# Kernel optimization log

Hardware: AMD Instinct MI355X
Metric: run time of the kernel (lower is better)

Reference implementation:

```python
import math
import jax, jax.numpy as jnp
import numpy as np
from jax import lax

SQRT2 = 1.4142135623730951
EPS = 1e-8


def _make_kernel():
    k = jnp.array([1.0, 3.0, 3.0, 1.0], jnp.float32)
    k = k[None, :] * k[:, None]
    return k / k.sum()  # [4,4], sums to 1


def _blur(x, kernel, pad, up=1):
    # upfirdn2d: optional zero-insertion upsample, pad, FIR filter (depthwise conv)
    C = x.shape[1]
    rhs = jnp.broadcast_to(kernel[None, None], (C, 1, kernel.shape[0], kernel.shape[1]))
    p0, p1 = pad
    if up > 1:
        p1 = p1 + (up - 1)  # zero-insertion appends up-1 trailing zeros per axis
    return lax.conv_general_dilated(
        x, rhs, (1, 1), [(p0, p1), (p0, p1)], lhs_dilation=(up, up),
        dimension_numbers=('NCHW', 'OIHW', 'NCHW'), feature_group_count=C)


def _mod_linear(style, mw, mb):
    # EqualLinear: scale = 1/sqrt(in_dim)
    scale = 1.0 / math.sqrt(mw.shape[1])
    return style @ (mw * scale).T + mb


def _mod_weight(w, s, demodulate):
    # w: [O,I,kh,kw], s: [B,I] -> per-sample weights [B,O,I,kh,kw]
    scale = 1.0 / math.sqrt(w.shape[1] * w.shape[2] * w.shape[3])
    wb = scale * w[None] * s[:, None, :, None, None]
    if demodulate:
        d = lax.rsqrt(jnp.sum(wb * wb, axis=(2, 3, 4)) + EPS)
        wb = wb * d[:, :, None, None, None]
    return wb


def _per_sample_conv(x, wb, padding):
    def f(xi, wi):
        return lax.conv_general_dilated(
            xi[None], wi, (1, 1), [(padding, padding)] * 2,
            dimension_numbers=('NCHW', 'OIHW', 'NCHW'))[0]
    return jax.vmap(f)(x, wb)


def _per_sample_conv_transpose2(x, wb):
    # torch conv_transpose2d(stride=2, pad=0) == lhs-dilated conv with flipped kernel
    k = wb.shape[-1]
    def f(xi, wi):
        return lax.conv_general_dilated(
            xi[None], jnp.flip(wi, (2, 3)), (1, 1), [(k - 1, k - 1)] * 2,
            lhs_dilation=(2, 2), dimension_numbers=('NCHW', 'OIHW', 'NCHW'))[0]
    return jax.vmap(f)(x, wb)


def _fused_lrelu(x, b):
    return jax.nn.leaky_relu(x + b[None, :, None, None], 0.2) * SQRT2


def setup_inputs() -> dict:
    key = jax.random.key(0)
    ks = jax.random.split(key, 16)
    B, C, H, S = 8, 512, 32, 512
    return {
        'x': jax.random.normal(ks[0], (B, C, H, H), jnp.float32),
        'style': jax.random.normal(ks[1], (B, S), jnp.float32),
        'skip_rgb': jax.random.normal(ks[2], (B, 3, H, H), jnp.float32),
        'noise1': jax.random.normal(ks[3], (B, 1, 2 * H, 2 * H), jnp.float32),
        'noise2': jax.random.normal(ks[4], (B, 1, 2 * H, 2 * H), jnp.float32),
        'w1': jax.random.normal(ks[5], (C, C, 3, 3), jnp.float32),
        'mod1_w': jax.random.normal(ks[6], (C, S), jnp.float32),
        'mod1_b': jnp.ones((C,), jnp.float32),
        'bias1': jnp.zeros((C,), jnp.float32),
        'noise1_w': 0.1 * jnp.ones((1,), jnp.float32),
        'w2': jax.random.normal(ks[7], (C, C, 3, 3), jnp.float32),
        'mod2_w': jax.random.normal(ks[8], (C, S), jnp.float32),
        'mod2_b': jnp.ones((C,), jnp.float32),
        'bias2': jnp.zeros((C,), jnp.float32),
        'noise2_w': 0.1 * jnp.ones((1,), jnp.float32),
        'w3': jax.random.normal(ks[9], (3, C, 1, 1), jnp.float32),
        'mod3_w': jax.random.normal(ks[10], (C, S), jnp.float32),
        'mod3_b': jnp.ones((C,), jnp.float32),
        'bias3': jnp.zeros((3,), jnp.float32),
    }


def reference(x, style, skip_rgb, noise1, noise2,
              w1, mod1_w, mod1_b, bias1, noise1_w,
              w2, mod2_w, mod2_b, bias2, noise2_w,
              w3, mod3_w, mod3_b, bias3):
    kernel = _make_kernel()
    # --- StyledConv with upsample: modulated conv_transpose + blur + noise + fused lrelu
    s1 = _mod_linear(style, mod1_w, mod1_b)            # [B, Cin]
    wb1 = _mod_weight(w1, s1, True)                    # [B, O, I, 3, 3]
    out = _per_sample_conv_transpose2(x, wb1)          # [B, O, 2H+1, 2W+1]
    out = _blur(out, kernel * 4.0, (1, 1))             # [B, O, 2H, 2W]
    out = out + noise1_w[0] * noise1
    out = _fused_lrelu(out, bias1)
    # --- StyledConv, same resolution
    s2 = _mod_linear(style, mod2_w, mod2_b)
    wb2 = _mod_weight(w2, s2, True)
    out = _per_sample_conv(out, wb2, 1)
    out = out + noise2_w[0] * noise2
    out = _fused_lrelu(out, bias2)
    # --- ToRGB: 1x1 modulated conv (no demodulation) + bias + upsampled skip
    s3 = _mod_linear(style, mod3_w, mod3_b)
    wb3 = _mod_weight(w3, s3, False)
    rgb = _per_sample_conv(out, wb3, 0) + bias3[None, :, None, None]
    skip = _blur(skip_rgb, kernel * 4.0, (2, 1), up=2)  # Upsample(factor=2)
    return rgb + skip
```

## Files before the change

### kernel.cpp

```cpp
#include <hip/hip_runtime.h>

typedef _Float16 f16;
typedef __attribute__((ext_vector_type(4))) _Float16 f16x4;
typedef __attribute__((ext_vector_type(8))) _Float16 f16x8;
typedef __attribute__((ext_vector_type(4))) float f32x4;

#define SC_CONV 0.014731391274719738f
#define SC_RGB  0.04419417382415922f
#define SC_LIN  0.04419417382415922f
#define SQRT2F  1.4142135623730951f

__device__ inline f32x4 zero_f32x4() {
    f32x4 v;
    #pragma unroll
    for (int i = 0; i < 4; ++i) v[i] = 0.0f;
    return v;
}
__device__ inline void gload_lds16(const void* g, void* l) {
    __builtin_amdgcn_global_load_lds(
        (const __attribute__((address_space(1))) unsigned int*)g,
        (__attribute__((address_space(3))) unsigned int*)l, 16, 0, 0);
}

__global__ __launch_bounds__(256) void k_prep1(
    const float* __restrict__ style,
    const float* __restrict__ m1w, const float* __restrict__ m1b,
    const float* __restrict__ m2w, const float* __restrict__ m2b,
    const float* __restrict__ m3w, const float* __restrict__ m3b,
    float* __restrict__ s1, float* __restrict__ s2, float* __restrict__ s3,
    const float* __restrict__ w1, const float* __restrict__ w2,
    f16* __restrict__ wA1, f16* __restrict__ wA2,
    float* __restrict__ wsq1, float* __restrict__ wsq2,
    f16* __restrict__ xmh, f16* __restrict__ in1h, f16* __restrict__ ctp,
    const float* __restrict__ skiprgb, const float* __restrict__ bias3,
    float* __restrict__ out)
{
    const int bx = blockIdx.x;
    if (bx < 2048) {
        int g = bx * 256 + threadIdx.x;
        int set = g >> 18; int oi = g & 262143;
        const float* w = (set ? w2 : w1) + (size_t)oi * 9;
        f16* wa = set ? wA2 : wA1;
        float* wq = set ? wsq2 : wsq1;
        int o = oi >> 9, i = oi & 511;
        float sw = 0.f;
        #pragma unroll
        for (int t = 0; t < 9; ++t) {
            float v = w[t];
            wa[((size_t)t * 512 + o) * 512 + i] = (f16)v;
            sw += v * v;
        }
        wq[oi] = sw;
    } else if (bx < 2432) {
        const int lane = threadIdx.x & 63, wid = threadIdx.x >> 6;
        const int gw = (bx - 2048) * 4 + wid;
        const int set = gw >> 9, o = gw & 511;
        const float* mw = set == 0 ? m1w : set == 1 ? m2w : m3w;
        const float* mb = set == 0 ? m1b : set == 1 ? m2b : m3b;
        float* outp = set == 0 ? s1 : set == 1 ? s2 : s3;
        const float4 m0 = *(const float4*)(mw + (size_t)o * 512 + lane * 8);
        const float4 m1 = *(const float4*)(mw + (size_t)o * 512 + lane * 8 + 4);
        const float mv[8] = {m0.x, m0.y, m0.z, m0.w, m1.x, m1.y, m1.z, m1.w};
        float acc[8];
        #pragma unroll
        for (int b = 0; b < 8; ++b) {
            const float4 sA = *(const float4*)(style + b * 512 + lane * 8);
            const float4 sB = *(const float4*)(style + b * 512 + lane * 8 + 4);
            acc[b] = mv[0]*sA.x + mv[1]*sA.y + mv[2]*sA.z + mv[3]*sA.w
                   + mv[4]*sB.x + mv[5]*sB.y + mv[6]*sB.z + mv[7]*sB.w;
        }
        #pragma unroll
        for (int b = 0; b < 8; ++b)
            #pragma unroll
            for (int off = 1; off < 64; off <<= 1)
                acc[b] += __shfl_xor(acc[b], off);
        if (lane == 0) {
            const float mbv = mb[o];
            #pragma unroll
            for (int b = 0; b < 8; ++b) outp[b * 512 + o] = acc[b] * SC_LIN + mbv;
        }
    } else if (bx < 2448) {
        const int idx = bx - 2432, b = idx & 7, type = idx >> 3;
        f16x8 z;
        #pragma unroll
        for (int i = 0; i < 8; ++i) z[i] = (_Float16)0.0f;
        if (type == 0) {
            for (int j = threadIdx.x; j < 132 * 64; j += 256) {
                int pix = j >> 6, e = j & 63;
                int r, c;
                if (pix < 34)       { r = 0;            c = pix; }
                else if (pix < 68)  { r = 33;           c = pix - 34; }
                else if (pix < 100) { r = pix - 68 + 1; c = 0; }
                else                { r = pix - 100 + 1; c = 33; }
                *(f16x8*)(xmh + ((((size_t)b * 34 + r) * 34 + c) * 512) + e * 8) = z;
            }
        } else {
            for (int j = threadIdx.x; j < 260 * 64; j += 256) {
                int pix = j >> 6, e = j & 63;
                int r, c;
                if (pix < 66)       { r = 0;             c = pix; }
                else if (pix < 132) { r = 65;            c = pix - 66; }
                else if (pix < 196) { r = pix - 132 + 1; c = 0; }
                else                { r = pix - 196 + 1; c = 65; }
                *(f16x8*)(in1h + ((((size_t)b * 66 + r) * 66 + c) * 512) + e * 8) = z;
            }
        }
    } else if (bx < 2456) {
        const int b = bx - 2448;
        f16x8 z;
        #pragma unroll
        for (int i = 0; i < 8; ++i) z[i] = (_Float16)0.0f;
        for (int j = threadIdx.x; j < 266 * 64; j += 256) {
            int pix = j >> 6, e = j & 63;
            int r, c;
            if (pix < 68)       { r = 0;             c = pix; }
            else if (pix < 136) { r = 66;            c = pix - 68; }
            else if (pix < 201) { r = 1 + (pix - 136); c = 0; }
            else                { r = 1 + (pix - 201); c = 66; }
            *(f16x8*)(ctp + ((((size_t)b * 68 + r) * 68 + c) * 512) + e * 8) = z;
        }
    } else {
        const unsigned g = (unsigned)(bx - 2456) * 256 + threadIdx.x;
        const unsigned b = g / 12288u, rem = g - b * 12288u;
        const unsigned c = rem >> 12, pix = rem & 4095u;
        const int y = (int)(pix >> 6), xx = (int)(pix & 63);
        const float kk[4] = {1.f, 3.f, 3.f, 1.f};
        int sy = y & 1, sx = xx & 1;
        int u0 = ((y + sy) >> 1) - 1, v0 = ((xx + sx) >> 1) - 1;
        float cy0 = kk[sy], cy1 = kk[sy + 2], cx0 = kk[sx], cx1 = kk[sx + 2];
        float sk = 0.f;
        #pragma unroll
        for (int aa = 0; aa < 2; ++aa)
            #pragma unroll
            for (int bb = 0; bb < 2; ++bb) {
                int u = u0 + aa, vv = v0 + bb;
                if (u >= 0 && u < 32 && vv >= 0 && vv < 32)
                    sk += (aa ? cy1 : cy0) * (bb ? cx1 : cx0) *
                          skiprgb[(((size_t)b * 3 + c) * 32 + u) * 32 + vv];
            }
        out[(((size_t)b * 3 + c) * 64 + y) * 64 + xx] = bias3[c] + sk * (1.0f / 16.0f);
    }
}

__global__ __launch_bounds__(256) void k_prep2(
    const float* __restrict__ wsq1, const float* __restrict__ s1, float* __restrict__ d1,
    const float* __restrict__ wsq2, const float* __restrict__ s2, float* __restrict__ d2,
    const float* __restrict__ x, f16* __restrict__ xmh)
{
    __shared__ float red[8][4];
    __shared__ float t[32][33];
    const int bx = blockIdx.x;
    if (bx < 1024) {
        const int o = bx & 511, set = bx >> 9;
        const float* wq = set ? wsq2 : wsq1;
        const float* s = set ? s2 : s1;
        float* d = set ? d2 : d1;
        float acc[8] = {0,0,0,0,0,0,0,0};
        for (int i = threadIdx.x; i < 512; i += 256) {
            const float sw = wq[(size_t)o * 512 + i];
            #pragma unroll
            for (int b = 0; b < 8; ++b) { float sv = s[b * 512 + i]; acc[b] += sv * sv * sw; }
        }
        const int lane = threadIdx.x & 63, wid = threadIdx.x >> 6;
        #pragma unroll
        for (int b = 0; b < 8; ++b)
            #pragma unroll
            for (int off = 1; off < 64; off <<= 1)
                acc[b] += __shfl_xor(acc[b], off);
        if (lane == 0) {
            #pragma unroll
            for (int b = 0; b < 8; ++b) red[b][wid] = acc[b];
        }
        __syncthreads();
        if (threadIdx.x < 8) {
            float s4 = red[threadIdx.x][0] + red[threadIdx.x][1] + red[threadIdx.x][2] + red[threadIdx.x][3];
            d[threadIdx.x * 512 + o] = rsqrtf(s4 * (SC_CONV * SC_CONV) + 1e-8f);
        }
    } else {
        const int idx = bx - 1024, u = idx & 31, b = idx >> 5;
        int tx = threadIdx.x & 31, ty = threadIdx.x >> 5;
        for (int ic = 0; ic < 512; ic += 32) {
            #pragma unroll
            for (int k = 0; k < 4; ++k) {
                int i = ic + ty + 8 * k;
                t[ty + 8 * k][tx] = x[(((size_t)b * 512 + i) * 32 + u) * 32 + tx];
            }
            __syncthreads();
            #pragma unroll
            for (int k = 0; k < 4; ++k) {
                int v = ty + 8 * k;
                int i = ic + tx;
                float sv = s1[b * 512 + i] * SC_CONV;
                xmh[(((size_t)b * 34 + u + 1) * 34 + v + 1) * 512 + i] = (f16)(t[tx][v] * sv);
            }
            __syncthreads();
        }
    }
}

__global__ __launch_bounds__(512, 2) void k_conv1m(
    const f16* __restrict__ xmh, const f16* __restrict__ wA1, f16* __restrict__ ctp)
{
    const int gid = blockIdx.x;
    int ph, tbase;
    if (gid < 70)       { ph = 0; tbase = 0; }
    else if (gid < 136) { ph = 1; tbase = 70; }
    else if (gid < 202) { ph = 2; tbase = 136; }
    else                { ph = 3; tbase = 202; }
    const int p = ph >> 1, q = ph & 1;
    const int Nn = q ? 32 : 33;
    const unsigned npos = (unsigned)((p ? 32 : 33) * Nn);
    const unsigned ntot = npos * 8;
    const int tiles_n = (int)((ntot + 255) >> 8);
    int t = gid - tbase;
    const int mB = (t >= tiles_n) ? 256 : 0;
    if (t >= tiles_n) t -= tiles_n;
    const unsigned posB = (unsigned)t * 256;
    const int ntx = q ? 1 : 2;
    const int ntaps = (p ? 1 : 2) * ntx;
    const int ktsteps = ntaps * 8;

    __shared__ f16 LA[2][16384];
    __shared__ f16 LB[2][16384];
    const int tid = threadIdx.x, lane = tid & 63, wid = tid >> 6;
    const int wm = wid >> 2, wn = wid & 3;
    const int lr = lane & 15, lk = lane >> 4;

    f32x4 acc[8][4];
    #pragma unroll
    for (int mf = 0; mf < 8; ++mf)
        #pragma unroll
        for (int nf = 0; nf < 4; ++nf) acc[mf][nf] = zero_f32x4();

    int aoff[4], boff[4], ldst[4];
    #pragma unroll
    for (int c = 0; c < 4; ++c) {
        const int idx = c * 512 + tid;
        const int row = idx >> 3, sl = idx & 7, ssl = sl ^ (row & 7);
        ldst[c] = idx * 16;
        aoff[c] = (mB + row) * 512 + ssl * 8;
        unsigned pos = posB + (unsigned)row;
        if (pos > ntot - 1) pos = ntot - 1;
        const unsigned bb = pos / npos, rr = pos - bb * npos;
        const unsigned u = rr / (unsigned)Nn, v = rr - u * (unsigned)Nn;
        boff[c] = (int)(((bb * 34 + u + 1) * 34 + v + 1) * 512) + ssl * 8;
    }

    int raA[8], raB[4];
    #pragma unroll
    for (int mf = 0; mf < 8; ++mf) {
        const int R = wm * 128 + mf * 16 + lr;
        raA[mf] = R * 128 + ((lk ^ (R & 7)) * 16);
    }
    #pragma unroll
    for (int nf = 0; nf < 4; ++nf) {
        const int R = wn * 64 + nf * 16 + lr;
        raB[nf] = R * 128 + ((lk ^ (R & 7)) * 16);
    }

    auto stageA = [&](int kt, int d) {
        const int tt = kt >> 3, icb = (kt & 7) << 6;
        const int ay = (ntx == 2) ? (tt >> 1) : tt;
        const int ax = (ntx == 2) ? (tt & 1) : 0;
        const f16* base = wA1 + (size_t)((p + 2 * ay) * 3 + (q + 2 * ax)) * 262144 + icb;
        char* dst = (char*)LA[d];
        #pragma unroll
        for (int c = 0; c < 4; ++c)
            gload_lds16(base + aoff[c], dst + ldst[c]);
    };
    auto stageB = [&](int kt, int d) {
        const int tt = kt >> 3, icb = (kt & 7) << 6;
        const int ay = (ntx == 2) ? (tt >> 1) : tt;
        const int ax = (ntx == 2) ? (tt & 1) : 0;
        const f16* base = xmh - (long)(ay * 34 + ax) * 512 + icb;
        char* dst = (char*)LB[d];
        #pragma unroll
        for (int c = 0; c < 4; ++c)
            gload_lds16(base + boff[c], dst + ldst[c]);
    };

    stageB(0, 0);
    stageA(0, 0);
    for (int kt = 0; kt < ktsteps; ++kt) {
        const int d = kt & 1;
        asm volatile("s_waitcnt vmcnt(0)" ::: "memory");
        __builtin_amdgcn_s_barrier();
        const char* A = (const char*)LA[d];
        const char* Bm = (const char*)LB[d];
        f16x8 bf[4][2], af[4][2];
        #pragma unroll
        for (int nf = 0; nf < 4; ++nf) {
            bf[nf][0] = *(const f16x8*)(Bm + raB[nf]);
            bf[nf][1] = *(const f16x8*)(Bm + (raB[nf] ^ 64));
        }
        #pragma unroll
        for (int mf = 0; mf < 4; ++mf) {
            af[mf][0] = *(const f16x8*)(A + raA[mf]);
            af[mf][1] = *(const f16x8*)(A + (raA[mf] ^ 64));
        }
        if (kt + 1 < ktsteps) stageB(kt + 1, d ^ 1);
        asm volatile("s_waitcnt lgkmcnt(0)" ::: "memory");
        __builtin_amdgcn_sched_barrier(0);
        __builtin_amdgcn_s_setprio(1);
        #pragma unroll
        for (int mf = 0; mf < 4; ++mf)
            #pragma unroll
            for (int nf = 0; nf < 4; ++nf) {
                acc[mf][nf] = __builtin_amdgcn_mfma_f32_16x16x32_f16(
                    af[mf][0], bf[nf][0], acc[mf][nf], 0, 0, 0);
                acc[mf][nf] = __builtin_amdgcn_mfma_f32_16x16x32_f16(
                    af[mf][1], bf[nf][1], acc[mf][nf], 0, 0, 0);
            }
        __builtin_amdgcn_s_setprio(0);
        #pragma unroll
        for (int mf = 0; mf < 4; ++mf) {
            af[mf][0] = *(const f16x8*)(A + raA[mf + 4]);
            af[mf][1] = *(const f16x8*)(A + (raA[mf + 4] ^ 64));
        }
        if (kt + 1 < ktsteps) stageA(kt + 1, d ^ 1);
        asm volatile("s_waitcnt lgkmcnt(0)" ::: "memory");
        __builtin_amdgcn_sched_barrier(0);
        __builtin_amdgcn_s_setprio(1);
        #pragma unroll
        for (int mf = 0; mf < 4; ++mf)
            #pragma unroll
            for (int nf = 0; nf < 4; ++nf) {
                acc[mf + 4][nf] = __builtin_amdgcn_mfma_f32_16x16x32_f16(
                    af[mf][0], bf[nf][0], acc[mf + 4][nf], 0, 0, 0);
                acc[mf + 4][nf] = __builtin_amdgcn_mfma_f32_16x16x32_f16(
                    af[mf][1], bf[nf][1], acc[mf + 4][nf], 0, 0, 0);
            }
        __builtin_amdgcn_s_setprio(0);
    }

    #pragma unroll
    for (int nf = 0; nf < 4; ++nf) {
        const int c = wn * 64 + nf * 16 + lr;
        const unsigned pos = posB + (unsigned)c;
        if (pos >= ntot) continue;
        const unsigned bb = pos / npos, rr = pos - bb * npos;
        const unsigned u = rr / (unsigned)Nn, v = rr - u * (unsigned)Nn;
        const int row = 1 + 2 * (int)u + p, col = 1 + 2 * (int)v + q;
        f16* dst = ctp + (((size_t)bb * 68 + row) * 68 + col) * 512;
        #pragma unroll
        for (int mf = 0; mf < 8; ++mf) {
            const int ob = mB + wm * 128 + mf * 16 + lk * 4;
            f16x4 st;
            #pragma unroll
            for (int r = 0; r < 4; ++r) st[r] = (f16)acc[mf][nf][r];
            *(f16x4*)(dst + ob) = st;
        }
    }
}

__global__ __launch_bounds__(256) void k_blur1(
    const f16* __restrict__ ctp, const float* __restrict__ d1,
    const float* __restrict__ noise1, const float* __restrict__ nw1,
    const float* __restrict__ bias1, const float* __restrict__ s2,
    f16* __restrict__ in1h)
{
    const int y0 = blockIdx.x * 2, b = blockIdx.y;
    const int tx = threadIdx.x & 63, xg = threadIdx.x >> 6;
    const int ch = tx * 8, x0 = xg * 16;
    const f16* base = ctp + ((size_t)(b * 68 + y0) * 68) * 512 + ch;

    float d1v[8], b1v[8], s2v[8];
    {
        const float4 a0 = *(const float4*)(d1 + b * 512 + ch);
        const float4 a1 = *(const float4*)(d1 + b * 512 + ch + 4);
        const float4 c0 = *(const float4*)(bias1 + ch);
        const float4 c1 = *(const float4*)(bias1 + ch + 4);
        const float4 e0 = *(const float4*)(s2 + b * 512 + ch);
        const float4 e1 = *(const float4*)(s2 + b * 512 + ch + 4);
        d1v[0]=a0.x; d1v[1]=a0.y; d1v[2]=a0.z; d1v[3]=a0.w;
        d1v[4]=a1.x; d1v[5]=a1.y; d1v[6]=a1.z; d1v[7]=a1.w;
        b1v[0]=c0.x; b1v[1]=c0.y; b1v[2]=c0.z; b1v[3]=c0.w;
        b1v[4]=c1.x; b1v[5]=c1.y; b1v[6]=c1.z; b1v[7]=c1.w;
        s2v[0]=e0.x; s2v[1]=e0.y; s2v[2]=e0.z; s2v[3]=e0.w;
        s2v[4]=e1.x; s2v[5]=e1.y; s2v[6]=e1.z; s2v[7]=e1.w;
    }
    const float nw = nw1[0];
    const float* nrow0 = noise1 + ((size_t)b * 64 + y0) * 64;
    const float* nrow1 = nrow0 + 64;

    float cs[4][2][8];
    #define LOADCOL(cc, slot)                                                   \
        do {                                                                    \
            f16x8 v0 = *(const f16x8*)(base + ((size_t)(0 * 68 + (cc))) * 512); \
            f16x8 v1 = *(const f16x8*)(base + ((size_t)(1 * 68 + (cc))) * 512); \
            f16x8 v2 = *(const f16x8*)(base + ((size_t)(2 * 68 + (cc))) * 512); \
            f16x8 v3 = *(const f16x8*)(base + ((size_t)(3 * 68 + (cc))) * 512); \
            f16x8 v4 = *(const f16x8*)(base + ((size_t)(4 * 68 + (cc))) * 512); \
            _Pragma("unroll")                                                   \
            for (int k = 0; k < 8; ++k) {                                       \
                float f0=(float)v0[k], f1=(float)v1[k], f2=(float)v2[k];        \
                float f3=(float)v3[k], f4=(float)v4[k];                         \
                cs[slot][0][k] = f0 + 3.f*f1 + 3.f*f2 + f3;                     \
                cs[slot][1][k] = f1 + 3.f*f2 + 3.f*f3 + f4;                     \
            }                                                                   \
        } while (0)

    LOADCOL(x0 + 0, 0);
    LOADCOL(x0 + 1, 1);
    LOADCOL(x0 + 2, 2);
    #pragma unroll
    for (int xi = 0; xi < 16; ++xi) {
        LOADCOL(x0 + xi + 3, ((xi + 3) & 3));
        const int x = x0 + xi;
        const float nz0 = nw * nrow0[x];
        const float nz1 = nw * nrow1[x];
        f16x8 st0, st1;
        #pragma unroll
        for (int k = 0; k < 8; ++k) {
            float s0 = (cs[xi & 3][0][k] + cs[(xi + 3) & 3][0][k])
                     + 3.f * (cs[(xi + 1) & 3][0][k] + cs[(xi + 2) & 3][0][k]);
            float v0 = s0 * (1.0f / 16.0f) * d1v[k] + nz0 + b1v[k];
            v0 = (v0 > 0.f ? v0 : 0.2f * v0) * SQRT2F;
            st0[k] = (f16)(v0 * s2v[k] * SC_CONV);
            float s1r = (cs[xi & 3][1][k] + cs[(xi + 3) & 3][1][k])
                      + 3.f * (cs[(xi + 1) & 3][1][k] + cs[(xi + 2) & 3][1][k]);
            float v1 = s1r * (1.0f / 16.0f) * d1v[k] + nz1 + b1v[k];
            v1 = (v1 > 0.f ? v1 : 0.2f * v1) * SQRT2F;
            st1[k] = (f16)(v1 * s2v[k] * SC_CONV);
        }
        *(f16x8*)(in1h + (((size_t)(b * 66 + 1 + y0) * 66) + 1 + x) * 512 + ch) = st0;
        *(f16x8*)(in1h + (((size_t)(b * 66 + 2 + y0) * 66) + 1 + x) * 512 + ch) = st1;
    }
    #undef LOADCOL
}

__global__ __launch_bounds__(512, 2) void k_conv2_8p(
    const f16* __restrict__ in1h, const f16* __restrict__ wA2,
    const float* __restrict__ d2, const float* __restrict__ noise2,
    const float* __restrict__ nw2, const float* __restrict__ bias2,
    const float* __restrict__ s3, const float* __restrict__ w3,
    float* __restrict__ out)
{
    const int b = blockIdx.z, mB = blockIdx.y * 256, nT = blockIdx.x;
    const int y0 = nT * 4;
    __shared__ f16 LA[2][16384];
    __shared__ f16 LB[2][16384];
    const int tid = threadIdx.x, lane = tid & 63, wid = tid >> 6;
    const int wm = wid >> 2, wn = wid & 3;
    const int lr = lane & 15, lk = lane >> 4;

    f32x4 acc[8][4];
    #pragma unroll
    for (int mf = 0; mf < 8; ++mf)
        #pragma unroll
        for (int nf = 0; nf < 4; ++nf) acc[mf][nf] = zero_f32x4();

    int aoff[4], boff[4], ldst[4];
    #pragma unroll
    for (int c = 0; c < 4; ++c) {
        const int idx = c * 512 + tid;
        const int row = idx >> 3, sl = idx & 7, ssl = sl ^ (row & 7);
        ldst[c] = idx * 16;
        aoff[c] = (mB + row) * 512 + ssl * 8;
        const int py = y0 + (row >> 6), px = row & 63;
        boff[c] = ((b * 66 + 1 + py) * 66 + 1 + px) * 512 + ssl * 8;
    }

    int raA[8], raB[4];
    #pragma unroll
    for (int mf = 0; mf < 8; ++mf) {
        const int R = wm * 128 + mf * 16 + lr;
        raA[mf] = R * 128 + ((lk ^ (R & 7)) * 16);
    }
    #pragma unroll
    for (int nf = 0; nf < 4; ++nf) {
        const int R = wn * 64 + nf * 16 + lr;
        raB[nf] = R * 128 + ((lk ^ (R & 7)) * 16);
    }

    auto stageA = [&](int kt, int d) {
        const int tap = kt >> 3, icb = (kt & 7) << 6;
        const f16* base = wA2 + (size_t)tap * 262144 + icb;
        char* dst = (char*)LA[d];
        #pragma unroll
        for (int c = 0; c < 4; ++c)
            gload_lds16(base + aoff[c], dst + ldst[c]);
    };
    auto stageB = [&](int kt, int d) {
        const int tap = kt >> 3, icb = (kt & 7) << 6;
        const int dy = tap / 3 - 1, dx = tap - (tap / 3) * 3 - 1;
        const f16* base = in1h + (dy * 66 + dx) * 512 + icb;
        char* dst = (char*)LB[d];
        #pragma unroll
        for (int c = 0; c < 4; ++c)
            gload_lds16(base + boff[c], dst + ldst[c]);
    };

    stageB(0, 0);
    stageA(0, 0);
    for (int kt = 0; kt < 72; ++kt) {
        const int d = kt & 1;
        asm volatile("s_waitcnt vmcnt(0)" ::: "memory");
        __builtin_amdgcn_s_barrier();
        const char* A = (const char*)LA[d];
        const char* Bm = (const char*)LB[d];
        f16x8 bf[4][2], af[4][2];
        #pragma unroll
        for (int nf = 0; nf < 4; ++nf) {
            bf[nf][0] = *(const f16x8*)(Bm + raB[nf]);
            bf[nf][1] = *(const f16x8*)(Bm + (raB[nf] ^ 64));
        }
        #pragma unroll
        for (int mf = 0; mf < 4; ++mf) {
            af[mf][0] = *(const f16x8*)(A + raA[mf]);
            af[mf][1] = *(const f16x8*)(A + (raA[mf] ^ 64));
        }
        if (kt + 1 < 72) stageB(kt + 1, d ^ 1);
        asm volatile("s_waitcnt lgkmcnt(0)" ::: "memory");
        __builtin_amdgcn_sched_barrier(0);
        __builtin_amdgcn_s_setprio(1);
        #pragma unroll
        for (int mf = 0; mf < 4; ++mf)
            #pragma unroll
            for (int nf = 0; nf < 4; ++nf) {
                acc[mf][nf] = __builtin_amdgcn_mfma_f32_16x16x32_f16(
                    af[mf][0], bf[nf][0], acc[mf][nf], 0, 0, 0);
                acc[mf][nf] = __builtin_amdgcn_mfma_f32_16x16x32_f16(
                    af[mf][1], bf[nf][1], acc[mf][nf], 0, 0, 0);
            }
        __builtin_amdgcn_s_setprio(0);
        #pragma unroll
        for (int mf = 0; mf < 4; ++mf) {
            af[mf][0] = *(const f16x8*)(A + raA[mf + 4]);
            af[mf][1] = *(const f16x8*)(A + (raA[mf + 4] ^ 64));
        }
        if (kt + 1 < 72) stageA(kt + 1, d ^ 1);
        asm volatile("s_waitcnt lgkmcnt(0)" ::: "memory");
        __builtin_amdgcn_sched_barrier(0);
        __builtin_amdgcn_s_setprio(1);
        #pragma unroll
        for (int mf = 0; mf < 4; ++mf)
            #pragma unroll
            for (int nf = 0; nf < 4; ++nf) {
                acc[mf + 4][nf] = __builtin_amdgcn_mfma_f32_16x16x32_f16(
                    af[mf][0], bf[nf][0], acc[mf + 4][nf], 0, 0, 0);
                acc[mf + 4][nf] = __builtin_amdgcn_mfma_f32_16x16x32_f16(
                    af[mf][1], bf[nf][1], acc[mf + 4][nf], 0, 0, 0);
            }
        __builtin_amdgcn_s_setprio(0);
    }

    const float* d2b = d2 + b * 512;
    const float* s3b = s3 + b * 512;
    const float nw = nw2[0];
    float p3[4][3];
    #pragma unroll
    for (int nf = 0; nf < 4; ++nf)
        #pragma unroll
        for (int c = 0; c < 3; ++c) p3[nf][c] = 0.f;
    #pragma unroll
    for (int mf = 0; mf < 8; ++mf) {
        const int ob = mB + wm * 128 + mf * 16 + lk * 4;
        const float4 dv = *(const float4*)(d2b + ob);
        const float4 bv = *(const float4*)(bias2 + ob);
        const float4 sv = *(const float4*)(s3b + ob);
        const float4 w0 = *(const float4*)(w3 + 0 * 512 + ob);
        const float4 w1v = *(const float4*)(w3 + 1 * 512 + ob);
        const float4 w2v = *(const float4*)(w3 + 2 * 512 + ob);
        const float dd[4] = {dv.x, dv.y, dv.z, dv.w};
        const float bb[4] = {bv.x, bv.y, bv.z, bv.w};
        const float ss[4] = {sv.x, sv.y, sv.z, sv.w};
        const float w0r[4] = {w0.x, w0.y, w0.z, w0.w};
        const float w1r[4] = {w1v.x, w1v.y, w1v.z, w1v.w};
        const float w2r[4] = {w2v.x, w2v.y, w2v.z, w2v.w};
        #pragma unroll
        for (int nf = 0; nf < 4; ++nf) {
            const int c = wn * 64 + nf * 16 + lr;
            const int py = y0 + (c >> 6), px = c & 63;
            const float nz = nw * noise2[((size_t)b * 64 + py) * 64 + px];
            #pragma unroll
            for (int r = 0; r < 4; ++r) {
                float v = acc[mf][nf][r] * dd[r] + nz + bb[r];
                v = (v > 0.f ? v : 0.2f * v) * SQRT2F;
                v *= ss[r] * SC_RGB;
                p3[nf][0] += v * w0r[r];
                p3[nf][1] += v * w1r[r];
                p3[nf][2] += v * w2r[r];
            }
        }
    }
    #pragma unroll
    for (int nf = 0; nf < 4; ++nf)
        #pragma unroll
        for (int c = 0; c < 3; ++c) {
            float v = p3[nf][c];
            v += __shfl_xor(v, 16);
            v += __shfl_xor(v, 32);
            p3[nf][c] = v;
        }
    if (lk == 0) {
        #pragma unroll
        for (int nf = 0; nf < 4; ++nf) {
            const int c = wn * 64 + nf * 16 + lr;
            const int py = y0 + (c >> 6), px = c & 63;
            #pragma unroll
            for (int ch = 0; ch < 3; ++ch)
                atomicAdd(out + (((size_t)b * 3 + ch) * 64 + py) * 64 + px, p3[nf][ch]);
        }
    }
}

extern "C" void kernel_launch(void* const* d_in, const int* in_sizes, int n_in,
                              void* d_out, int out_size, void* d_ws, size_t ws_size,
                              hipStream_t stream)
{
    const float* x       = (const float*)d_in[0];
    const float* style   = (const float*)d_in[1];
    const float* skiprgb = (const float*)d_in[2];
    const float* noise1  = (const float*)d_in[3];
    const float* noise2  = (const float*)d_in[4];
    const float* w1      = (const float*)d_in[5];
    const float* m1w     = (const float*)d_in[6];
    const float* m1b     = (const float*)d_in[7];
    const float* bias1   = (const float*)d_in[8];
    const float* nw1     = (const float*)d_in[9];
    const float* w2      = (const float*)d_in[10];
    const float* m2w     = (const float*)d_in[11];
    const float* m2b     = (const float*)d_in[12];
    const float* bias2   = (const float*)d_in[13];
    const float* nw2     = (const float*)d_in[14];
    const float* w3      = (const float*)d_in[15];
    const float* m3w     = (const float*)d_in[16];
    const float* m3b     = (const float*)d_in[17];
    const float* bias3   = (const float*)d_in[18];
    float* out = (float*)d_out;

    char* p = (char*)d_ws;
    auto alloc = [&](size_t bytes) { char* r = p; p += (bytes + 255) & ~(size_t)255; return r; };
    float* s1 = (float*)alloc(8 * 512 * 4);
    float* s2 = (float*)alloc(8 * 512 * 4);
    float* s3 = (float*)alloc(8 * 512 * 4);
    float* d1 = (float*)alloc(8 * 512 * 4);
    float* d2 = (float*)alloc(8 * 512 * 4);
    float* wsq1 = (float*)alloc((size_t)512 * 512 * 4);
    float* wsq2 = (float*)alloc((size_t)512 * 512 * 4);
    f16* wA1 = (f16*)alloc((size_t)9 * 512 * 512 * 2);
    f16* wA2 = (f16*)alloc((size_t)9 * 512 * 512 * 2);
    const size_t XMH_B  = (size_t)8 * 34 * 34 * 512 * 2;
    const size_t CTP_B  = (size_t)8 * 68 * 68 * 512 * 2;
    const size_t IN1H_B = (size_t)8 * 66 * 66 * 512 * 2;
    char* ovl = (char*)alloc(XMH_B + CTP_B + IN1H_B);
    f16* xmh  = (f16*)ovl;
    f16* ctp  = (f16*)(ovl + XMH_B);
    f16* in1h = (f16*)(ovl + XMH_B + CTP_B);

    k_prep1<<<2840, 256, 0, stream>>>(style, m1w, m1b, m2w, m2b, m3w, m3b, s1, s2, s3,
                                      w1, w2, wA1, wA2, wsq1, wsq2, xmh, in1h, ctp,
                                      skiprgb, bias3, out);
    k_prep2<<<1280, 256, 0, stream>>>(wsq1, s1, d1, wsq2, s2, d2, x, xmh);
    k_conv1m<<<266, 512, 0, stream>>>(xmh, wA1, ctp);
    k_blur1<<<dim3(32, 8), 256, 0, stream>>>(ctp, d1, noise1, nw1, bias1, s2, in1h);
    k_conv2_8p<<<dim3(16, 2, 8), 512, 0, stream>>>(in1h, wA2, d2, noise2, nw2, bias2, s3, w3, out);
}
```

Baseline: 246.3 us.

## Split conv2 K-tiles into half-depth stages with partial vmcnt waits

```diff
diff --git a/kernel.cpp b/kernel.cpp
--- a/kernel.cpp
+++ b/kernel.cpp
@@ -438,8 +438,8 @@
 {
     const int b = blockIdx.z, mB = blockIdx.y * 256, nT = blockIdx.x;
     const int y0 = nT * 4;
-    __shared__ f16 LA[2][16384];
-    __shared__ f16 LB[2][16384];
+    __shared__ f16 LA[4][8192];
+    __shared__ f16 LB[4][8192];
     const int tid = threadIdx.x, lane = tid & 63, wid = tid >> 6;
     const int wm = wid >> 2, wn = wid & 3;
     const int lr = lane & 15, lk = lane >> 4;
@@ -450,100 +450,77 @@
         #pragma unroll
         for (int nf = 0; nf < 4; ++nf) acc[mf][nf] = zero_f32x4();
 
-    int aoff[4], boff[4], ldst[4];
-    #pragma unroll
-    for (int c = 0; c < 4; ++c) {
+    int aoff[2], boff[2], ldst[2];
+    #pragma unroll
+    for (int c = 0; c < 2; ++c) {
         const int idx = c * 512 + tid;
-        const int row = idx >> 3, sl = idx & 7, ssl = sl ^ (row & 7);
+        const int row = idx >> 2, sl = idx & 3;
+        const int ks = sl ^ ((row >> 1) & 3);
         ldst[c] = idx * 16;
-        aoff[c] = (mB + row) * 512 + ssl * 8;
+        aoff[c] = (mB + row) * 512 + ks * 8;
         const int py = y0 + (row >> 6), px = row & 63;
-        boff[c] = ((b * 66 + 1 + py) * 66 + 1 + px) * 512 + ssl * 8;
+        boff[c] = ((b * 66 + 1 + py) * 66 + 1 + px) * 512 + ks * 8;
     }
 
     int raA[8], raB[4];
     #pragma unroll
     for (int mf = 0; mf < 8; ++mf) {
         const int R = wm * 128 + mf * 16 + lr;
-        raA[mf] = R * 128 + ((lk ^ (R & 7)) * 16);
+        raA[mf] = R * 64 + ((lk ^ ((R >> 1) & 3)) * 16);
     }
     #pragma unroll
     for (int nf = 0; nf < 4; ++nf) {
         const int R = wn * 64 + nf * 16 + lr;
-        raB[nf] = R * 128 + ((lk ^ (R & 7)) * 16);
-    }
-
-    auto stageA = [&](int kt, int d) {
-        const int tap = kt >> 3, icb = (kt & 7) << 6;
-        const f16* base = wA2 + (size_t)tap * 262144 + icb;
-        char* dst = (char*)LA[d];
-        #pragma unroll
-        for (int c = 0; c < 4; ++c)
-            gload_lds16(base + aoff[c], dst + ldst[c]);
+        raB[nf] = R * 64 + ((lk ^ ((R >> 1) & 3)) * 16);
+    }
+
+    auto stage = [&](int kt, int h) {
+        const int d = kt & 1;
+        const int tap = kt >> 3, icb = ((kt & 7) << 6) + h * 32;
+        const f16* Ab = wA2 + (size_t)tap * 262144 + icb;
+        const int dy = tap / 3 - 1, dx = tap - (tap / 3) * 3 - 1;
+        const f16* Bb = in1h + (dy * 66 + dx) * 512 + icb;
+        char* Ad = (char*)LA[d * 2 + h];
+        char* Bd = (char*)LB[d * 2 + h];
+        gload_lds16(Ab + aoff[0], Ad + ldst[0]);
+        gload_lds16(Ab + aoff[1], Ad + ldst[1]);
+        gload_lds16(Bb + boff[0], Bd + ldst[0]);
+        gload_lds16(Bb + boff[1], Bd + ldst[1]);
     };
-    auto stageB = [&](int kt, int d) {
-        const int tap = kt >> 3, icb = (kt & 7) << 6;
-        const int dy = tap / 3 - 1, dx = tap - (tap / 3) * 3 - 1;
-        const f16* base = in1h + (dy * 66 + dx) * 512 + icb;
-        char* dst = (char*)LB[d];
-        #pragma unroll
-        for (int c = 0; c < 4; ++c)
-            gload_lds16(base + boff[c], dst + ldst[c]);
-    };
-
-    stageB(0, 0);
-    stageA(0, 0);
-    for (int kt = 0; kt < 72; ++kt) {
+
+    auto phase = [&](int kt, int h, bool doStage, int vm) {
+        if (vm == 4) asm volatile("s_waitcnt vmcnt(4)" ::: "memory");
+        else         asm volatile("s_waitcnt vmcnt(0)" ::: "memory");
+        __builtin_amdgcn_s_barrier();
         const int d = kt & 1;
-        asm volatile("s_waitcnt vmcnt(0)" ::: "memory");
-        __builtin_amdgcn_s_barrier();
-        const char* A = (const char*)LA[d];
-        const char* Bm = (const char*)LB[d];
-        f16x8 bf[4][2], af[4][2];
-        #pragma unroll
-        for (int nf = 0; nf < 4; ++nf) {
-            bf[nf][0] = *(const f16x8*)(Bm + raB[nf]);
-            bf[nf][1] = *(const f16x8*)(Bm + (raB[nf] ^ 64));
-        }
-        #pragma unroll
-        for (int mf = 0; mf < 4; ++mf) {
-            af[mf][0] = *(const f16x8*)(A + raA[mf]);
-            af[mf][1] = *(const f16x8*)(A + (raA[mf] ^ 64));
-        }
-        if (kt + 1 < 72) stageB(kt + 1, d ^ 1);
+        const char* A  = (const char*)LA[d * 2 + h];
+        const char* Bm = (const char*)LB[d * 2 + h];
+        f16x8 af[8], bf[4];
+        #pragma unroll
+        for (int nf = 0; nf < 4; ++nf) bf[nf] = *(const f16x8*)(Bm + raB[nf]);
+        #pragma unroll
+        for (int mf = 0; mf < 8; ++mf) af[mf] = *(const f16x8*)(A + raA[mf]);
+        if (doStage) stage(kt + 1, h);
         asm volatile("s_waitcnt lgkmcnt(0)" ::: "memory");
         __builtin_amdgcn_sched_barrier(0);
         __builtin_amdgcn_s_setprio(1);
         #pragma unroll
-        for (int mf = 0; mf < 4; ++mf)
-            #pragma unroll
-            for (int nf = 0; nf < 4; ++nf) {
+        for (int mf = 0; mf < 8; ++mf)
+            #pragma unroll
+            for (int nf = 0; nf < 4; ++nf)
                 acc[mf][nf] = __builtin_amdgcn_mfma_f32_16x16x32_f16(
-                    af[mf][0], bf[nf][0], acc[mf][nf], 0, 0, 0);
-                acc[mf][nf] = __builtin_amdgcn_mfma_f32_16x16x32_f16(
-                    af[mf][1], bf[nf][1], acc[mf][nf], 0, 0, 0);
-            }
+                    af[mf], bf[nf], acc[mf][nf], 0, 0, 0);
         __builtin_amdgcn_s_setprio(0);
-        #pragma unroll
-        for (int mf = 0; mf < 4; ++mf) {
-            af[mf][0] = *(const f16x8*)(A + raA[mf + 4]);
-            af[mf][1] = *(const f16x8*)(A + (raA[mf + 4] ^ 64));
-        }
-        if (kt + 1 < 72) stageA(kt + 1, d ^ 1);
-        asm volatile("s_waitcnt lgkmcnt(0)" ::: "memory");
-        __builtin_amdgcn_sched_barrier(0);
-        __builtin_amdgcn_s_setprio(1);
-        #pragma unroll
-        for (int mf = 0; mf < 4; ++mf)
-            #pragma unroll
-            for (int nf = 0; nf < 4; ++nf) {
-                acc[mf + 4][nf] = __builtin_amdgcn_mfma_f32_16x16x32_f16(
-                    af[mf][0], bf[nf][0], acc[mf + 4][nf], 0, 0, 0);
-                acc[mf + 4][nf] = __builtin_amdgcn_mfma_f32_16x16x32_f16(
-                    af[mf][1], bf[nf][1], acc[mf + 4][nf], 0, 0, 0);
-            }
-        __builtin_amdgcn_s_setprio(0);
-    }
+    };
+
+    stage(0, 0);
+    stage(0, 1);
+    for (int kt = 0; kt < 71; ++kt) {
+        phase(kt, 0, true, 4);
+        phase(kt, 1, true, 4);
+    }
+    phase(71, 0, false, 4);
+    phase(71, 1, false, 0);
 
     const float* d2b = d2 + b * 512;
     const float* s3b = s3 + b * 512;
```

New measurement: 253.2 us. +2.8%, slower.
